# Performance work log

Hardware: AMD Instinct MI355X
Metric: run time of the kernel (lower is better)

The kernel has to match this reference:

```python
import jax, jax.numpy as jnp
import numpy as np

INPUT_DIM = 512
DEGREE = 3
NUM_KNOTS = 16
NUM_NEURONS = 1024
OUTPUT_DIM = 512
NUM_BASIS = NUM_KNOTS + DEGREE - 1  # 18


def make_knots():
    # uniform grid on [0,1], extended by `degree` knots on each side
    h = 1.0 / (NUM_KNOTS - 1)
    grid = np.linspace(0.0, 1.0, NUM_KNOTS)
    lo = grid[0] - h * np.arange(DEGREE, 0, -1)
    hi = grid[-1] + h * np.arange(1, DEGREE + 1)
    return jnp.asarray(np.concatenate([lo, grid, hi]), dtype=jnp.float32)  # [NUM_KNOTS+2*DEGREE]


def bspline_basis(x, t, degree):
    # x: [B, N]; t: [K] uniform extended knots. Cox-de Boor recursion.
    K = t.shape[0]
    xb = x[..., None]
    B = ((xb >= t[:-1]) & (xb < t[1:])).astype(x.dtype)  # [B, N, K-1]
    for p in range(1, degree + 1):
        ti = t[: K - p - 1]
        tip = t[p : K - 1]
        ti1 = t[1 : K - p]
        tip1 = t[p + 1 : K]
        left = (xb - ti) / (tip - ti) * B[..., :-1]
        right = (tip1 - xb) / (tip1 - ti1) * B[..., 1:]
        B = left + right
    return B  # [B, N, K-1-degree] == [B, N, NUM_BASIS]


def norm_layer(x, eps=1e-8):
    # per-row min-max normalization into the spline domain [0,1)
    mn = jnp.min(x, axis=-1, keepdims=True)
    mx = jnp.max(x, axis=-1, keepdims=True)
    return (x - mn) / (mx - mn + eps)


def setup_inputs() -> dict:
    key = jax.random.key(0)
    ks = jax.random.split(key, 7)
    x = jax.random.normal(ks[0], (4096, INPUT_DIM), dtype=jnp.float32)
    s1 = 1.0 / np.sqrt(INPUT_DIM)
    s2 = 1.0 / np.sqrt(NUM_NEURONS)
    W1 = jax.random.uniform(ks[1], (INPUT_DIM, NUM_NEURONS), jnp.float32, -s1, s1)
    b1 = jax.random.uniform(ks[2], (NUM_NEURONS,), jnp.float32, -s1, s1)
    coeff = jax.random.normal(ks[3], (NUM_NEURONS, NUM_BASIS), dtype=jnp.float32) * 0.1
    sp_bias = jnp.zeros((NUM_NEURONS,), dtype=jnp.float32)
    W2 = jax.random.uniform(ks[4], (NUM_NEURONS, OUTPUT_DIM), jnp.float32, -s2, s2)
    b2 = jax.random.uniform(ks[5], (OUTPUT_DIM,), jnp.float32, -s2, s2)
    return {"x": x, "W1": W1, "b1": b1, "coeff": coeff, "sp_bias": sp_bias, "W2": W2, "b2": b2}


def reference(x, W1, b1, coeff, sp_bias, W2, b2):
    t = make_knots()
    h = x @ W1 + b1                      # [B, N]  Linear 1
    h = norm_layer(h)                    # NormLayer -> [0,1)
    basis = bspline_basis(h, t, DEGREE)  # [B, N, NUM_BASIS]
    sp = jnp.einsum('bnk,nk->bn', basis, coeff) + sp_bias  # per-neuron spline eval
    out = sp @ W2 + b2                   # Linear 2
    return jax.nn.relu(out)
```

## Files before the change

kernel.cpp:

```cpp
#include <hip/hip_runtime.h>

#define M_ROWS  4096
#define IN_DIM  512
#define NEURONS 1024
#define OUT_DIM 512

typedef _Float16 f16;
typedef __attribute__((ext_vector_type(8))) _Float16 f16x8;
typedef __attribute__((ext_vector_type(4))) _Float16 f16x4;
typedef __attribute__((ext_vector_type(4))) float    f32x4;

__global__ __launch_bounds__(256) void prep(
    const float* __restrict__ x,  f16* __restrict__ xh,
    const float* __restrict__ W1, f16* __restrict__ W1t,
    const float* __restrict__ W2, f16* __restrict__ W2t,
    const float* __restrict__ coeff, const float* __restrict__ spb,
    f16* __restrict__ cpH)
{
    __shared__ float S[32][33];
    const int b = blockIdx.x, t = threadIdx.x;
    if (b < 1024) {
        int i = b * 256 + t;
        const float4* p = (const float4*)x;
        float4 a = p[i * 2], c = p[i * 2 + 1];
        f16x8 o = { (f16)a.x, (f16)a.y, (f16)a.z, (f16)a.w,
                    (f16)c.x, (f16)c.y, (f16)c.z, (f16)c.w };
        *(f16x8*)(xh + (size_t)i * 8) = o;
        return;
    }
    if (b < 1536) {
        const int tile = b - 1024;
        const int tx = tile & 31, ty = tile >> 5;
        const int tr = t >> 3, tc = (t & 7) * 4;
        float4 v = *(const float4*)&W1[(size_t)(ty * 32 + tr) * NEURONS + tx * 32 + tc];
        S[tr][tc + 0] = v.x; S[tr][tc + 1] = v.y;
        S[tr][tc + 2] = v.z; S[tr][tc + 3] = v.w;
        __syncthreads();
        f16x4 o = {(f16)S[tc + 0][tr], (f16)S[tc + 1][tr],
                   (f16)S[tc + 2][tr], (f16)S[tc + 3][tr]};
        *(f16x4*)&W1t[(size_t)(tx * 32 + tr) * IN_DIM + ty * 32 + tc] = o;
        return;
    }
    if (b < 2048) {
        const int tile = b - 1536;
        const int nt = tile & 15, kt2 = tile >> 4;
        const int tr = t >> 3, tc = (t & 7) * 4;
        float4 v = *(const float4*)&W2[(size_t)(kt2 * 32 + tr) * OUT_DIM + nt * 32 + tc];
        S[tr][tc + 0] = v.x; S[tr][tc + 1] = v.y;
        S[tr][tc + 2] = v.z; S[tr][tc + 3] = v.w;
        __syncthreads();
        const int n = nt * 32 + tr;
        f16x4 o = {(f16)S[tc + 0][tr], (f16)S[tc + 1][tr],
                   (f16)S[tc + 2][tr], (f16)S[tc + 3][tr]};
        const int kbyte = ((kt2 * 32 + tc) * 2) ^ ((n & 7) << 4);
        *(f16x4*)((char*)W2t + (size_t)n * 2048 + kbyte) = o;
        return;
    }
    {
        const int tid = (b - 2048) * 256 + t;
        if (tid < NEURONS * 15) {
            const int n = tid / 15, ii = tid % 15;
            const float s = spb[n];
            f16x4 c;
            c[0] = (f16)(coeff[n * 18 + ii]     + s);
            c[1] = (f16)(coeff[n * 18 + ii + 1] + s);
            c[2] = (f16)(coeff[n * 18 + ii + 2] + s);
            c[3] = (f16)(coeff[n * 18 + ii + 3] + s);
            *(f16x4*)&cpH[(size_t)tid * 4] = c;
        }
    }
}

__global__ __launch_bounds__(256) void k_gemm1(
    const f16* __restrict__ A, const f16* __restrict__ Bt,
    const float* __restrict__ b1, f16* __restrict__ h,
    float* __restrict__ pmin, float* __restrict__ pmax)
{
    __shared__ f16 lds[2][(128 + 64) * 64];

    const int t    = threadIdx.x;
    const int lane = t & 63, l15 = lane & 15, lhi = lane >> 4;
    const int wid  = t >> 6;
    const int wm   = wid >> 1, wn = wid & 1;

    const int flat = blockIdx.y * gridDim.x + blockIdx.x;
    const int swz  = (flat & 7) * 64 + (flat >> 3);
    const int m0   = (swz >> 4) * 128;
    const int n0   = (swz & 15) * 64;

    auto stage = [&](int buf, int kt) {
        f16* base = &lds[buf][0];
#pragma unroll
        for (int j = 0; j < 4; ++j) {
            int c = wid * 4 + j;
            const f16* g = A + (size_t)(m0 + c * 8 + (lane >> 3)) * IN_DIM + kt + (lane & 7) * 8;
            __builtin_amdgcn_global_load_lds(
                (const __attribute__((address_space(1))) void*)g,
                (__attribute__((address_space(3))) void*)(base + c * 512), 16, 0, 0);
        }
#pragma unroll
        for (int j = 0; j < 2; ++j) {
            int c = wid * 2 + j;
            const f16* g = Bt + (size_t)(n0 + c * 8 + (lane >> 3)) * IN_DIM + kt + (lane & 7) * 8;
            __builtin_amdgcn_global_load_lds(
                (const __attribute__((address_space(1))) void*)g,
                (__attribute__((address_space(3))) void*)(base + 8192 + c * 512), 16, 0, 0);
        }
    };

    f32x4 acc[4][2];
#pragma unroll
    for (int i = 0; i < 4; ++i)
#pragma unroll
        for (int j = 0; j < 2; ++j) acc[i][j] = (f32x4)0.f;

    stage(0, 0);
    __syncthreads();

    int cur = 0;
    for (int tt = 0; tt < 8; ++tt) {
        if (tt < 7) stage(cur ^ 1, (tt + 1) * 64);
        const f16* L = &lds[cur][0];
#pragma unroll
        for (int ks = 0; ks < 2; ++ks) {
            f16x8 bfr[2];
#pragma unroll
            for (int nj = 0; nj < 2; ++nj)
                bfr[nj] = *(const f16x8*)
                    &L[8192 + (wn * 32 + nj * 16 + l15) * 64 + ks * 32 + lhi * 8];
#pragma unroll
            for (int mi = 0; mi < 4; ++mi) {
                f16x8 afr = *(const f16x8*)
                    &L[(wm * 64 + mi * 16 + l15) * 64 + ks * 32 + lhi * 8];
#pragma unroll
                for (int nj = 0; nj < 2; ++nj)
                    acc[mi][nj] = __builtin_amdgcn_mfma_f32_16x16x32_f16(
                        afr, bfr[nj], acc[mi][nj], 0, 0, 0);
            }
        }
        __syncthreads();
        cur ^= 1;
    }

    const int nb2 = (n0 >> 6) * 2 + wn;
#pragma unroll
    for (int mi = 0; mi < 4; ++mi) {
        const int row0 = m0 + wm * 64 + mi * 16 + lhi * 4;
        float vmn[4], vmx[4];
#pragma unroll
        for (int nj = 0; nj < 2; ++nj) {
            const int col = n0 + wn * 32 + nj * 16 + l15;
            const float bv = b1[col];
#pragma unroll
            for (int j = 0; j < 4; ++j) {
                f16 hv = (f16)(acc[mi][nj][j] + bv);
                h[(size_t)(row0 + j) * NEURONS + col] = hv;
                float vr = (float)hv;
                if (nj == 0) { vmn[j] = vr; vmx[j] = vr; }
                else { vmn[j] = fminf(vmn[j], vr); vmx[j] = fmaxf(vmx[j], vr); }
            }
        }
#pragma unroll
        for (int j = 0; j < 4; ++j) {
#pragma unroll
            for (int d = 1; d < 16; d <<= 1) {
                vmn[j] = fminf(vmn[j], __shfl_xor(vmn[j], d));
                vmx[j] = fmaxf(vmx[j], __shfl_xor(vmx[j], d));
            }
        }
        if (l15 == 0) {
#pragma unroll
            for (int j = 0; j < 4; ++j) {
                pmin[(size_t)nb2 * M_ROWS + row0 + j] = vmn[j];
                pmax[(size_t)nb2 * M_ROWS + row0 + j] = vmx[j];
            }
        }
    }
}

__global__ __launch_bounds__(256) void sp_gemm2(
    const f16* __restrict__ h, const float* __restrict__ pmin,
    const float* __restrict__ pmax, const f16* __restrict__ cpH,
    const f16* __restrict__ W2t, const float* __restrict__ b2,
    float* __restrict__ out)
{
    __shared__ __align__(16) f16 Bb[512 * 64];
    __shared__ __align__(16) f16 Aa[2][16 * 72];
    __shared__ __align__(16) f16 cpS[2][4096];
    __shared__ float red[2][16][17];
    __shared__ float mnS[16], inv15S[16];

    const int t    = threadIdx.x;
    const int lane = t & 63, l15 = lane & 15, lhi = lane >> 4;
    const int wid  = t >> 6;

    const int flat = blockIdx.x;
    const int swz  = (flat & 7) * 32 + (flat >> 3);
    const int m0   = swz * 16;

    auto stageB = [&](int s) {
        char* base = (char*)&Bb[0];
#pragma unroll
        for (int j = 0; j < 16; ++j) {
            const int r = wid * 128 + j * 8 + (lane >> 3);
            const char* src = (const char*)W2t + (size_t)r * 2048
                              + s * 128 + (lane & 7) * 16;
            __builtin_amdgcn_global_load_lds(
                (const __attribute__((address_space(1))) void*)src,
                (__attribute__((address_space(3))) void*)(base + (size_t)r * 128
                                                          + (lane & 7) * 16 - (size_t)(lane & 7) * 16
                                                          + (wid * 128 + j * 8) * 128),
                0, 0, 0);
        }
    };
    (void)stageB;

    auto stageB2 = [&](int s) {
        char* base = (char*)&Bb[0];
#pragma unroll
        for (int j = 0; j < 16; ++j) {
            const int rg = wid * 128 + j * 8;
            const char* src = (const char*)W2t + (size_t)(rg + (lane >> 3)) * 2048
                              + s * 128 + (lane & 7) * 16;
            __builtin_amdgcn_global_load_lds(
                (const __attribute__((address_space(1))) void*)src,
                (__attribute__((address_space(3))) void*)(base + (size_t)rg * 128),
                16, 0, 0);
        }
    };
    auto stageCp = [&](int s) {
        const char* src = (const char*)cpH + (size_t)s * 7680 + t * 16;
        char* base = (char*)&cpS[s & 1][0];
        __builtin_amdgcn_global_load_lds(
            (const __attribute__((address_space(1))) void*)(src),
            (__attribute__((address_space(3))) void*)(base + (t >> 6) * 1024), 16, 0, 0);
        __builtin_amdgcn_global_load_lds(
            (const __attribute__((address_space(1))) void*)(src + 4096),
            (__attribute__((address_space(3))) void*)(base + 4096 + (t >> 6) * 1024), 16, 0, 0);
    };

    const int sr_ = t >> 4;
    const int skc = (t & 15) * 4;
    auto loadH = [&](int s) -> f16x4 {
        return *(const f16x4*)&h[(size_t)(m0 + sr_) * NEURONS + s * 64 + skc];
    };
    auto splineA = [&](int s, f16x4 hv) {
        const float mn = mnS[sr_], inv15 = inv15S[sr_];
        const f16* cps = &cpS[s & 1][0];
        f16x4 o;
#pragma unroll
        for (int e = 0; e < 4; ++e) {
            const float t15 = ((float)hv[e] - mn) * inv15;
            int ii = (int)t15;
            ii = ii < 0 ? 0 : (ii > 14 ? 14 : ii);
            const float tl  = t15 - (float)ii;
            const float t2  = tl * tl, t3 = t2 * tl;
            const float omt = 1.0f - tl;
            const float b0  = omt * omt * omt * (1.0f / 6.0f);
            const float b3v = t3 * (1.0f / 6.0f);
            const float b1v = (4.0f / 6.0f) - t2 + 0.5f * t3;
            const float b2v = (1.0f / 6.0f) + 0.5f * (tl + t2 - t3);
            const f16x4 c   = *(const f16x4*)&cps[((skc + e) * 15 + ii) * 4];
            o[e] = (f16)((float)c[0] * b0 + (float)c[1] * b1v
                       + (float)c[2] * b2v + (float)c[3] * b3v);
        }
        *(f16x4*)&Aa[s & 1][sr_ * 72 + skc] = o;
    };

    stageCp(0); stageCp(1); stageB2(0);
    {
        const int r_ = t & 15, p = t >> 4;
        const int row = m0 + r_;
        red[0][r_][p] = fminf(pmin[(size_t)p * M_ROWS + row],
                              pmin[(size_t)(p + 16) * M_ROWS + row]);
        red[1][r_][p] = fmaxf(pmax[(size_t)p * M_ROWS + row],
                              pmax[(size_t)(p + 16) * M_ROWS + row]);
    }
    __syncthreads();
    if (t < 16) {
        float a = red[0][t][0], b = red[1][t][0];
#pragma unroll
        for (int p = 1; p < 16; ++p) {
            a = fminf(a, red[0][t][p]);
            b = fmaxf(b, red[1][t][p]);
        }
        mnS[t] = a;
        inv15S[t] = 15.0f / (b - a + 1e-8f);
    }
    f16x4 hcur, hnext;
    hcur = loadH(0);
    hnext = loadH(1);
    __syncthreads();
    splineA(0, hcur);
    hcur = hnext;
    hnext = loadH(2);
    __syncthreads();

    f32x4 acc[8];
#pragma unroll
    for (int j = 0; j < 8; ++j) acc[j] = (f32x4)0.f;

    for (int s = 0; s < 16; ++s) {
#pragma unroll
        for (int ks = 0; ks < 2; ++ks) {
            f16x8 afr = *(const f16x8*)&Aa[s & 1][l15 * 72 + ks * 32 + lhi * 8];
#pragma unroll
            for (int nj = 0; nj < 8; ++nj) {
                const int cl = wid * 128 + nj * 16 + l15;
                const int kb = (ks * 64 + lhi * 16) ^ ((cl & 7) << 4);
                f16x8 bfr = *(const f16x8*)((const char*)&Bb[0] + (size_t)cl * 128 + kb);
                acc[nj] = __builtin_amdgcn_mfma_f32_16x16x32_f16(afr, bfr, acc[nj], 0, 0, 0);
            }
        }
        __syncthreads();
        if (s + 1 < 16) {
            stageB2(s + 1);
            if (s + 2 < 16) stageCp(s + 2);
            splineA(s + 1, hcur);
            hcur = hnext;
            if (s + 3 < 16) hnext = loadH(s + 3);
            __syncthreads();
        }
    }

    const int row0 = m0 + lhi * 4;
#pragma unroll
    for (int nj = 0; nj < 8; ++nj) {
        const int col = wid * 128 + nj * 16 + l15;
        const float bv = b2[col];
#pragma unroll
        for (int j = 0; j < 4; ++j)
            out[(size_t)(row0 + j) * OUT_DIM + col] =
                fmaxf(acc[nj][j] + bv, 0.0f);
    }
}

extern "C" void kernel_launch(void* const* d_in, const int* in_sizes, int n_in,
                              void* d_out, int out_size, void* d_ws, size_t ws_size,
                              hipStream_t stream)
{
    const float* x     = (const float*)d_in[0];
    const float* W1    = (const float*)d_in[1];
    const float* b1    = (const float*)d_in[2];
    const float* coeff = (const float*)d_in[3];
    const float* spb   = (const float*)d_in[4];
    const float* W2    = (const float*)d_in[5];
    const float* b2    = (const float*)d_in[6];
    float* out = (float*)d_out;

    char* ws = (char*)d_ws;
    f16*   h    = (f16*)ws;
    f16*   xh   = (f16*)(ws + ( 8u << 20));
    f16*   W1t  = (f16*)(ws + (12u << 20));
    f16*   W2t  = (f16*)(ws + (13u << 20));
    float* pmin = (float*)(ws + (14u << 20));
    float* pmax = (float*)(ws + (14u << 20) + (512u << 10));
    f16*   cpH  = (f16*)(ws + (15u << 20));

    prep<<<dim3(2108), 256, 0, stream>>>(x, xh, W1, W1t, W2, W2t, coeff, spb, cpH);

    k_gemm1<<<dim3(16, 32), 256, 0, stream>>>(xh, W1t, b1, h, pmin, pmax);

    sp_gemm2<<<dim3(256), 256, 0, stream>>>(h, pmin, pmax, cpH, W2t, b2, out);
}
```

Measured before the change: 52.18 us.

## Split gemm2 output columns across blocks and double-buffer B with one barrier

The spline+GEMM2 kernel now tiles the output as 16 rows by 256 columns, launching 512 blocks instead of 256. The K step drops from 64 to 32, and the W2 tile is double-buffered in LDS with a smaller swizzle, so there is one barrier per iteration instead of two. Prefetch and spline evaluation for the next step are issued before the MFMAs of the current step to overlap them. The cost is that each block redoes the spline evaluation for its rows, so that work doubles overall, and there are twice as many loop iterations.

```diff
diff --git a/kernel.cpp b/kernel.cpp
--- a/kernel.cpp
+++ b/kernel.cpp
@@ -8,6 +8,7 @@
 typedef _Float16 f16;
 typedef __attribute__((ext_vector_type(8))) _Float16 f16x8;
 typedef __attribute__((ext_vector_type(4))) _Float16 f16x4;
+typedef __attribute__((ext_vector_type(2))) _Float16 f16x2;
 typedef __attribute__((ext_vector_type(4))) float    f32x4;
 
 __global__ __launch_bounds__(256) void prep(
@@ -52,7 +53,7 @@
         const int n = nt * 32 + tr;
         f16x4 o = {(f16)S[tc + 0][tr], (f16)S[tc + 1][tr],
                    (f16)S[tc + 2][tr], (f16)S[tc + 3][tr]};
-        const int kbyte = ((kt2 * 32 + tc) * 2) ^ ((n & 7) << 4);
+        const int kbyte = ((kt2 * 32 + tc) * 2) ^ ((n & 3) << 4);
         *(f16x4*)((char*)W2t + (size_t)n * 2048 + kbyte) = o;
         return;
     }
@@ -184,9 +185,9 @@
     const f16* __restrict__ W2t, const float* __restrict__ b2,
     float* __restrict__ out)
 {
-    __shared__ __align__(16) f16 Bb[512 * 64];
-    __shared__ __align__(16) f16 Aa[2][16 * 72];
-    __shared__ __align__(16) f16 cpS[2][4096];
+    __shared__ __align__(16) f16 Bb[2][256 * 32];
+    __shared__ __align__(16) f16 Aa[2][16 * 40];
+    __shared__ __align__(16) f16 cpS[2][1920];
     __shared__ float red[2][16][17];
     __shared__ float mnS[16], inv15S[16];
 
@@ -195,61 +196,43 @@
     const int wid  = t >> 6;
 
     const int flat = blockIdx.x;
-    const int swz  = (flat & 7) * 32 + (flat >> 3);
-    const int m0   = swz * 16;
+    const int swz  = (flat & 7) * 64 + (flat >> 3);
+    const int m0   = (swz & 255) * 16;
+    const int n0   = (swz >> 8) * 256;
 
     auto stageB = [&](int s) {
-        char* base = (char*)&Bb[0];
-#pragma unroll
-        for (int j = 0; j < 16; ++j) {
-            const int r = wid * 128 + j * 8 + (lane >> 3);
-            const char* src = (const char*)W2t + (size_t)r * 2048
-                              + s * 128 + (lane & 7) * 16;
+        char* base = (char*)&Bb[s & 1][0];
+#pragma unroll
+        for (int j = 0; j < 4; ++j) {
+            const int rg = wid * 64 + j * 16;
+            const char* src = (const char*)W2t + (size_t)(n0 + rg + (lane >> 2)) * 2048
+                              + s * 64 + (lane & 3) * 16;
             __builtin_amdgcn_global_load_lds(
                 (const __attribute__((address_space(1))) void*)src,
-                (__attribute__((address_space(3))) void*)(base + (size_t)r * 128
-                                                          + (lane & 7) * 16 - (size_t)(lane & 7) * 16
-                                                          + (wid * 128 + j * 8) * 128),
-                0, 0, 0);
-        }
-    };
-    (void)stageB;
-
-    auto stageB2 = [&](int s) {
-        char* base = (char*)&Bb[0];
-#pragma unroll
-        for (int j = 0; j < 16; ++j) {
-            const int rg = wid * 128 + j * 8;
-            const char* src = (const char*)W2t + (size_t)(rg + (lane >> 3)) * 2048
-                              + s * 128 + (lane & 7) * 16;
+                (__attribute__((address_space(3))) void*)(base + rg * 64), 16, 0, 0);
+        }
+    };
+    auto stageCp = [&](int s) {
+        if (t < 240) {
+            const char* src = (const char*)cpH + (size_t)s * 3840 + t * 16;
+            char* base = (char*)&cpS[s & 1][0] + wid * 1024;
             __builtin_amdgcn_global_load_lds(
                 (const __attribute__((address_space(1))) void*)src,
-                (__attribute__((address_space(3))) void*)(base + (size_t)rg * 128),
-                16, 0, 0);
-        }
-    };
-    auto stageCp = [&](int s) {
-        const char* src = (const char*)cpH + (size_t)s * 7680 + t * 16;
-        char* base = (char*)&cpS[s & 1][0];
-        __builtin_amdgcn_global_load_lds(
-            (const __attribute__((address_space(1))) void*)(src),
-            (__attribute__((address_space(3))) void*)(base + (t >> 6) * 1024), 16, 0, 0);
-        __builtin_amdgcn_global_load_lds(
-            (const __attribute__((address_space(1))) void*)(src + 4096),
-            (__attribute__((address_space(3))) void*)(base + 4096 + (t >> 6) * 1024), 16, 0, 0);
+                (__attribute__((address_space(3))) void*)base, 16, 0, 0);
+        }
     };
 
     const int sr_ = t >> 4;
-    const int skc = (t & 15) * 4;
-    auto loadH = [&](int s) -> f16x4 {
-        return *(const f16x4*)&h[(size_t)(m0 + sr_) * NEURONS + s * 64 + skc];
-    };
-    auto splineA = [&](int s, f16x4 hv) {
+    const int skc = (t & 15) * 2;
+    auto loadH = [&](int s) -> f16x2 {
+        return *(const f16x2*)&h[(size_t)(m0 + sr_) * NEURONS + s * 32 + skc];
+    };
+    auto splineA = [&](int s, f16x2 hv) {
         const float mn = mnS[sr_], inv15 = inv15S[sr_];
         const f16* cps = &cpS[s & 1][0];
-        f16x4 o;
-#pragma unroll
-        for (int e = 0; e < 4; ++e) {
+        f16x2 o;
+#pragma unroll
+        for (int e = 0; e < 2; ++e) {
             const float t15 = ((float)hv[e] - mn) * inv15;
             int ii = (int)t15;
             ii = ii < 0 ? 0 : (ii > 14 ? 14 : ii);
@@ -264,10 +247,10 @@
             o[e] = (f16)((float)c[0] * b0 + (float)c[1] * b1v
                        + (float)c[2] * b2v + (float)c[3] * b3v);
         }
-        *(f16x4*)&Aa[s & 1][sr_ * 72 + skc] = o;
-    };
-
-    stageCp(0); stageCp(1); stageB2(0);
+        *(f16x2*)&Aa[s & 1][sr_ * 40 + skc] = o;
+    };
+
+    stageCp(0); stageCp(1); stageB(0);
     {
         const int r_ = t & 15, p = t >> 4;
         const int row = m0 + r_;
@@ -287,46 +270,43 @@
         mnS[t] = a;
         inv15S[t] = 15.0f / (b - a + 1e-8f);
     }
-    f16x4 hcur, hnext;
-    hcur = loadH(0);
-    hnext = loadH(1);
+    f16x2 hA = loadH(0);
     __syncthreads();
-    splineA(0, hcur);
-    hcur = hnext;
-    hnext = loadH(2);
+    splineA(0, hA);
+    hA = loadH(1);
+    f16x2 hB = loadH(2);
     __syncthreads();
 
-    f32x4 acc[8];
-#pragma unroll
-    for (int j = 0; j < 8; ++j) acc[j] = (f32x4)0.f;
-
-    for (int s = 0; s < 16; ++s) {
-#pragma unroll
-        for (int ks = 0; ks < 2; ++ks) {
-            f16x8 afr = *(const f16x8*)&Aa[s & 1][l15 * 72 + ks * 32 + lhi * 8];
-#pragma unroll
-            for (int nj = 0; nj < 8; ++nj) {
-                const int cl = wid * 128 + nj * 16 + l15;
-                const int kb = (ks * 64 + lhi * 16) ^ ((cl & 7) << 4);
-                f16x8 bfr = *(const f16x8*)((const char*)&Bb[0] + (size_t)cl * 128 + kb);
+    f32x4 acc[4];
+#pragma unroll
+    for (int j = 0; j < 4; ++j) acc[j] = (f32x4)0.f;
+
+    for (int s = 0; s < 32; ++s) {
+        if (s + 1 < 32) {
+            stageB(s + 1);
+            if (s + 2 < 32) stageCp(s + 2);
+            splineA(s + 1, hA);
+            hA = hB;
+            if (s + 3 < 32) hB = loadH(s + 3);
+        }
+        {
+            f16x8 afr = *(const f16x8*)&Aa[s & 1][l15 * 40 + lhi * 8];
+            const char* B_ = (const char*)&Bb[s & 1][0];
+#pragma unroll
+            for (int nj = 0; nj < 4; ++nj) {
+                const int cl = wid * 64 + nj * 16 + l15;
+                const int kb = (lhi * 16) ^ ((cl & 3) << 4);
+                f16x8 bfr = *(const f16x8*)(B_ + (size_t)cl * 64 + kb);
                 acc[nj] = __builtin_amdgcn_mfma_f32_16x16x32_f16(afr, bfr, acc[nj], 0, 0, 0);
             }
         }
         __syncthreads();
-        if (s + 1 < 16) {
-            stageB2(s + 1);
-            if (s + 2 < 16) stageCp(s + 2);
-            splineA(s + 1, hcur);
-            hcur = hnext;
-            if (s + 3 < 16) hnext = loadH(s + 3);
-            __syncthreads();
-        }
     }
 
     const int row0 = m0 + lhi * 4;
 #pragma unroll
-    for (int nj = 0; nj < 8; ++nj) {
-        const int col = wid * 128 + nj * 16 + l15;
+    for (int nj = 0; nj < 4; ++nj) {
+        const int col = n0 + wid * 64 + nj * 16 + l15;
         const float bv = b2[col];
 #pragma unroll
         for (int j = 0; j < 4; ++j)
@@ -361,5 +341,5 @@
 
     k_gemm1<<<dim3(16, 32), 256, 0, stream>>>(xh, W1t, b1, h, pmin, pmax);
 
-    sp_gemm2<<<dim3(256), 256, 0, stream>>>(h, pmin, pmax, cpH, W2t, b2, out);
+    sp_gemm2<<<dim3(512), 256, 0, stream>>>(h, pmin, pmax, cpH, W2t, b2, out);
 }
```

Measured after the change: 55.43 us. +6.2%, slower.
